# Kernel optimization log

Hardware: AMD Instinct MI355X
Metric: run time of the kernel (lower is better)

## Reference

```python
import jax, jax.numpy as jnp
import numpy as np

NEG_SLOPE = 0.2  # DGL GATConv default leaky_relu slope
N_LIG, E_LIG = 10000, 80000
N_REC, E_REC = 30000, 480000
B = 32  # graphs per batch


def setup_inputs() -> dict:
    key = jax.random.key(0)
    ks = jax.random.split(key, 32)
    d = {}
    d["x_lig"] = jax.random.normal(ks[0], (N_LIG, 64), jnp.float32)
    d["src_lig"] = jax.random.randint(ks[1], (E_LIG,), 0, N_LIG, jnp.int32)
    d["dst_lig"] = jax.random.randint(ks[2], (E_LIG,), 0, N_LIG, jnp.int32)
    d["gid_lig"] = jnp.sort(jax.random.randint(ks[3], (N_LIG,), 0, B, jnp.int32))
    d["x_rec"] = jax.random.normal(ks[4], (N_REC, 64), jnp.float32)
    d["src_rec"] = jax.random.randint(ks[5], (E_REC,), 0, N_REC, jnp.int32)
    d["dst_rec"] = jax.random.randint(ks[6], (E_REC,), 0, N_REC, jnp.int32)
    d["gid_rec"] = jnp.sort(jax.random.randint(ks[7], (N_REC,), 0, B, jnp.int32))
    s = 0.1
    # GAT layer 1 (lig): 64 -> 10 heads x 64 ; layer 2: 64 -> 1 head x 128
    d["W1l"] = s * jax.random.normal(ks[8], (64, 10 * 64), jnp.float32)
    d["al1l"] = s * jax.random.normal(ks[9], (10, 64), jnp.float32)
    d["ar1l"] = s * jax.random.normal(ks[10], (10, 64), jnp.float32)
    d["b1l"] = jnp.zeros((10, 64), jnp.float32)
    d["W2l"] = s * jax.random.normal(ks[11], (64, 128), jnp.float32)
    d["al2l"] = s * jax.random.normal(ks[12], (1, 128), jnp.float32)
    d["ar2l"] = s * jax.random.normal(ks[13], (1, 128), jnp.float32)
    d["b2l"] = jnp.zeros((1, 128), jnp.float32)
    d["W1r"] = s * jax.random.normal(ks[14], (64, 10 * 64), jnp.float32)
    d["al1r"] = s * jax.random.normal(ks[15], (10, 64), jnp.float32)
    d["ar1r"] = s * jax.random.normal(ks[16], (10, 64), jnp.float32)
    d["b1r"] = jnp.zeros((10, 64), jnp.float32)
    d["W2r"] = s * jax.random.normal(ks[17], (64, 128), jnp.float32)
    d["al2r"] = s * jax.random.normal(ks[18], (1, 128), jnp.float32)
    d["ar2r"] = s * jax.random.normal(ks[19], (1, 128), jnp.float32)
    d["b2r"] = jnp.zeros((1, 128), jnp.float32)
    d["W_lin1"] = s * jax.random.normal(ks[20], (256, 128), jnp.float32)
    d["b_lin1"] = jnp.zeros((128,), jnp.float32)
    d["W_lin2"] = s * jax.random.normal(ks[21], (128, 1), jnp.float32)
    d["b_lin2"] = jnp.zeros((1,), jnp.float32)
    return d


def gat_conv(x, src, dst, W, al, ar, b, num_nodes):
    # DGL GATConv (eval mode: dropouts off). al/ar: [H, D]
    H, D = al.shape
    h = (x @ W).reshape(num_nodes, H, D)          # [N, H, D]
    el = jnp.einsum("nhd,hd->nh", h, al)          # [N, H]
    er = jnp.einsum("nhd,hd->nh", h, ar)
    e = jax.nn.leaky_relu(el[src] + er[dst], NEG_SLOPE)   # [E, H]
    # edge softmax over incoming edges of each dst node
    emax = jax.ops.segment_max(e, dst, num_segments=num_nodes)
    ex = jnp.exp(e - emax[dst])
    denom = jax.ops.segment_sum(ex, dst, num_segments=num_nodes)
    alpha = ex / denom[dst]                       # [E, H]
    msg = alpha[:, :, None] * h[src]              # [E, H, D]
    out = jax.ops.segment_sum(msg, dst, num_segments=num_nodes)
    return out + b[None]                          # [N, H, D]


def branch(x, src, dst, gid, W1, al1, ar1, b1, W2, al2, ar2, b2):
    n = x.shape[0]
    h = jax.nn.relu(gat_conv(x, src, dst, W1, al1, ar1, b1, n)).sum(axis=1)  # sum heads -> [N, 64]
    h = jax.nn.relu(gat_conv(h, src, dst, W2, al2, ar2, b2, n))[:, 0, :]     # [N, 128]
    return jax.ops.segment_max(h, gid, num_segments=B)                       # max readout [B, 128]


def reference(x_lig, src_lig, dst_lig, gid_lig, x_rec, src_rec, dst_rec, gid_rec,
              W1l, al1l, ar1l, b1l, W2l, al2l, ar2l, b2l,
              W1r, al1r, ar1r, b1r, W2r, al2r, ar2r, b2r,
              W_lin1, b_lin1, W_lin2, b_lin2):
    hlig = branch(x_lig, src_lig, dst_lig, gid_lig, W1l, al1l, ar1l, b1l, W2l, al2l, ar2l, b2l)
    hrec = branch(x_rec, src_rec, dst_rec, gid_rec, W1r, al1r, ar1r, b1r, W2r, al2r, ar2r, b2r)
    h = jnp.concatenate([hlig, hrec], axis=-1)    # [B, 256]
    h = jax.nn.relu(h @ W_lin1 + b_lin1)
    h = jax.nn.relu(h @ W_lin2 + b_lin2)
    return h.flatten()                            # [B]
```

## Files before the change

### kernel.cpp

```cpp
#include <hip/hip_runtime.h>

#define LRELU(x) fmaxf((x), 0.2f*(x))
#define ZPAD(f) ((f) + 4*((f)>>6))

static inline int cdiv(int a, int b) { return (a + b - 1) / b; }

template<int H, int DH>
__global__ void prep_wal2_kernel(const float* __restrict__ WA, const float* __restrict__ alA,
                                 const float* __restrict__ arA, float* __restrict__ walA,
                                 float* __restrict__ warA, int nbA,
                                 const float* __restrict__ WB, const float* __restrict__ alB,
                                 const float* __restrict__ arB, float* __restrict__ walB,
                                 float* __restrict__ warB) {
  constexpr int K = 64;
  constexpr int HD = H * DH;
  const float *W, *al, *ar; float *wal, *war; int bid;
  if (blockIdx.x < (unsigned)nbA) { W=WA; al=alA; ar=arA; wal=walA; war=warA; bid=blockIdx.x; }
  else { W=WB; al=alB; ar=arB; wal=walB; war=warB; bid=blockIdx.x-nbA; }
  const int wv = threadIdx.x >> 6, lane = threadIdx.x & 63;
  const int o = bid * (blockDim.x >> 6) + wv;
  if (o >= H * K) return;
  const int h = o / K, k = o - h * K;
  float pl = 0.f, pr = 0.f;
#pragma unroll
  for (int j = 0; j < DH / 64; j++) {
    int d = j * 64 + lane;
    float w = W[(size_t)k * HD + h * DH + d];
    pl += w * al[h * DH + d];
    pr += w * ar[h * DH + d];
  }
#pragma unroll
  for (int off = 32; off >= 1; off >>= 1) {
    pl += __shfl_xor(pl, off);
    pr += __shfl_xor(pr, off);
  }
  if (lane == 0) { wal[o] = pl; war[o] = pr; }
}

__global__ void elr10_2_kernel(const float* __restrict__ xA, const float* __restrict__ walA,
                               const float* __restrict__ warA, float* __restrict__ elA,
                               float* __restrict__ erA, int NA, int nbA,
                               const float* __restrict__ xB, const float* __restrict__ walB,
                               const float* __restrict__ warB, float* __restrict__ elB,
                               float* __restrict__ erB, int NB) {
  const float *x, *wal, *war; float *el, *er; int N, bid;
  if (blockIdx.x < (unsigned)nbA) { x=xA; wal=walA; war=warA; el=elA; er=erA; N=NA; bid=blockIdx.x; }
  else { x=xB; wal=walB; war=warB; el=elB; er=erB; N=NB; bid=blockIdx.x-nbA; }
  const int wv = threadIdx.x >> 6, lane = threadIdx.x & 63;
  const int n = bid * (blockDim.x >> 6) + wv;
  if (n >= N) return;
  const float xv = x[(size_t)n * 64 + lane];
#pragma unroll
  for (int h = 0; h < 10; h++) {
    float pl = xv * wal[h * 64 + lane];
    float pr = xv * war[h * 64 + lane];
#pragma unroll
    for (int off = 32; off >= 1; off >>= 1) {
      pl += __shfl_xor(pl, off);
      pr += __shfl_xor(pr, off);
    }
    if (lane == 0) { el[(size_t)n * 10 + h] = pl; er[(size_t)n * 10 + h] = pr; }
  }
}

__global__ void deg2_kernel(const int* __restrict__ dstA, int* __restrict__ degA, int EA, int nbA,
                            const int* __restrict__ dstB, int* __restrict__ degB, int EB) {
  const int* dst; int* deg; int E, t;
  if (blockIdx.x < (unsigned)nbA) { dst=dstA; deg=degA; E=EA; t=blockIdx.x*256+threadIdx.x; }
  else { dst=dstB; deg=degB; E=EB; t=(blockIdx.x-nbA)*256+threadIdx.x; }
  if (t < E) atomicAdd(&deg[dst[t]], 1);
}

__global__ void rowptr2_kernel(const int* __restrict__ degA, int* __restrict__ rpA,
                               int* __restrict__ curA, int* __restrict__ cntA, int NA, int nbA,
                               const int* __restrict__ degB, int* __restrict__ rpB,
                               int* __restrict__ curB, int* __restrict__ cntB, int NB) {
  const int* deg; int *rp, *cur, *cnt; int N, t;
  if (blockIdx.x < (unsigned)nbA) { deg=degA; rp=rpA; cur=curA; cnt=cntA; N=NA; t=blockIdx.x*256+threadIdx.x; }
  else { deg=degB; rp=rpB; cur=curB; cnt=cntB; N=NB; t=(blockIdx.x-nbA)*256+threadIdx.x; }
  int lane = threadIdx.x & 63;
  int v = (t < N) ? deg[t] : 0;
  int x = v;
#pragma unroll
  for (int off = 1; off < 64; off <<= 1) {
    int y = __shfl_up(x, off);
    if (lane >= off) x += y;
  }
  int total = __shfl(x, 63);
  int base = 0;
  if (lane == 0 && total > 0) base = atomicAdd(cnt, total);
  base = __shfl(base, 0);
  int excl = base + x - v;
  if (t < N) { rp[t] = excl; cur[t] = excl; }
}

__global__ void scatter_ex2_kernel(
    const int* __restrict__ srcA, const int* __restrict__ dstA, int* __restrict__ curA,
    int* __restrict__ outA, const float* __restrict__ elA, const float* __restrict__ erA,
    float* __restrict__ exA, int EA, int nbA,
    const int* __restrict__ srcB, const int* __restrict__ dstB, int* __restrict__ curB,
    int* __restrict__ outB, const float* __restrict__ elB, const float* __restrict__ erB,
    float* __restrict__ exB, int EB) {
  const int *src, *dst; int *cur, *out; const float *el, *er; float *ex; int E, t;
  if (blockIdx.x < (unsigned)nbA) { src=srcA; dst=dstA; cur=curA; out=outA; el=elA; er=erA; ex=exA; E=EA; t=blockIdx.x*256+threadIdx.x; }
  else { src=srcB; dst=dstB; cur=curB; out=outB; el=elB; er=erB; ex=exB; E=EB; t=(blockIdx.x-nbA)*256+threadIdx.x; }
  if (t >= E) return;
  const int s = src[t], d = dst[t];
  const int slot = atomicAdd(&cur[d], 1);
  out[slot] = s;
  const float2* elv = (const float2*)el;
  const float2* erv = (const float2*)er;
  float2* exv = (float2*)ex;
#pragma unroll
  for (int j = 0; j < 5; j++) {
    float2 a = elv[(size_t)s * 5 + j];
    float2 b = erv[(size_t)d * 5 + j];
    float2 e;
    e.x = __expf(LRELU(a.x + b.x));
    e.y = __expf(LRELU(a.y + b.y));
    exv[(size_t)slot * 5 + j] = e;
  }
}

__global__ void aggr_z10_2_kernel(const int* __restrict__ rpA, const int* __restrict__ degA,
                                  const int* __restrict__ srcsA, const float* __restrict__ xA,
                                  const float* __restrict__ exA, float* __restrict__ zA,
                                  int NA, int nbA,
                                  const int* __restrict__ rpB, const int* __restrict__ degB,
                                  const int* __restrict__ srcsB, const float* __restrict__ xB,
                                  const float* __restrict__ exB, float* __restrict__ zB, int NB) {
  const int *rp, *degp, *srcs; const float *x, *ex; float *z; int N, bid;
  if (blockIdx.x < (unsigned)nbA) { rp=rpA; degp=degA; srcs=srcsA; x=xA; ex=exA; z=zA; N=NA; bid=blockIdx.x; }
  else { rp=rpB; degp=degB; srcs=srcsB; x=xB; ex=exB; z=zB; N=NB; bid=blockIdx.x-nbA; }
  const int wv = threadIdx.x >> 6, lane = threadIdx.x & 63;
  const int n = bid * (blockDim.x >> 6) + wv;
  if (n >= N) return;
  const int beg = rp[n], dg = degp[n];
  const float2* exv = (const float2*)ex;
  float den[10], acc[10];
#pragma unroll
  for (int h = 0; h < 10; h++) { den[h] = 0.f; acc[h] = 0.f; }
  int i = 0;
  for (; i + 1 < dg; i += 2) {
    int s0 = srcs[beg + i], s1 = srcs[beg + i + 1];
    float xv0 = x[(size_t)s0 * 64 + lane];
    float xv1 = x[(size_t)s1 * 64 + lane];
    float e0[10], e1[10];
#pragma unroll
    for (int j = 0; j < 5; j++) {
      float2 a = exv[(size_t)(beg + i) * 5 + j];
      float2 c = exv[(size_t)(beg + i + 1) * 5 + j];
      e0[2 * j] = a.x; e0[2 * j + 1] = a.y;
      e1[2 * j] = c.x; e1[2 * j + 1] = c.y;
    }
#pragma unroll
    for (int h = 0; h < 10; h++) {
      den[h] += e0[h] + e1[h];
      acc[h] = fmaf(e0[h], xv0, fmaf(e1[h], xv1, acc[h]));
    }
  }
  if (i < dg) {
    int s0 = srcs[beg + i];
    float xv0 = x[(size_t)s0 * 64 + lane];
#pragma unroll
    for (int j = 0; j < 5; j++) {
      float2 a = exv[(size_t)(beg + i) * 5 + j];
      den[2 * j] += a.x;
      den[2 * j + 1] += a.y;
      acc[2 * j] = fmaf(a.x, xv0, acc[2 * j]);
      acc[2 * j + 1] = fmaf(a.y, xv0, acc[2 * j + 1]);
    }
  }
#pragma unroll
  for (int h = 0; h < 10; h++)
    z[(size_t)n * 640 + h * 64 + lane] = (dg > 0) ? acc[h] / den[h] : 0.f;
}

__global__ void aggr_z1_2_kernel(const int* __restrict__ rpA, const int* __restrict__ degA,
                                 const int* __restrict__ srcsA, const float* __restrict__ hA,
                                 const float* __restrict__ elA, const float* __restrict__ erA,
                                 float* __restrict__ zA, int NA, int nbA,
                                 const int* __restrict__ rpB, const int* __restrict__ degB,
                                 const int* __restrict__ srcsB, const float* __restrict__ hB,
                                 const float* __restrict__ elB, const float* __restrict__ erB,
                                 float* __restrict__ zB, int NB) {
  const int *rp, *degp, *srcs; const float *hin, *el, *er; float *z; int N, bid;
  if (blockIdx.x < (unsigned)nbA) { rp=rpA; degp=degA; srcs=srcsA; hin=hA; el=elA; er=erA; z=zA; N=NA; bid=blockIdx.x; }
  else { rp=rpB; degp=degB; srcs=srcsB; hin=hB; el=elB; er=erB; z=zB; N=NB; bid=blockIdx.x-nbA; }
  const int wv = threadIdx.x >> 6, lane = threadIdx.x & 63;
  const int n = bid * (blockDim.x >> 6) + wv;
  if (n >= N) return;
  const int beg = rp[n], dg = degp[n];
  const float ern = er[n];
  float den = 0.f, acc = 0.f;
  int i = 0;
  for (; i + 1 < dg; i += 2) {
    int s0 = srcs[beg + i], s1 = srcs[beg + i + 1];
    float x0 = __expf(LRELU(el[s0] + ern));
    float x1 = __expf(LRELU(el[s1] + ern));
    den += x0 + x1;
    acc += x0 * hin[(size_t)s0 * 64 + lane] + x1 * hin[(size_t)s1 * 64 + lane];
  }
  if (i < dg) {
    int s0 = srcs[beg + i];
    float x0 = __expf(LRELU(el[s0] + ern));
    den += x0;
    acc += x0 * hin[(size_t)s0 * 64 + lane];
  }
  z[(size_t)n * 64 + lane] = (dg > 0) ? acc / den : 0.f;
}

__global__ void gemm_sumheads2_kernel(
    const float* __restrict__ zA, const float* __restrict__ WA, const float* __restrict__ bA,
    const float* __restrict__ wal2A, const float* __restrict__ war2A, float* __restrict__ h1A,
    float* __restrict__ el2A, float* __restrict__ er2A, int NA, int nbA,
    const float* __restrict__ zB, const float* __restrict__ WB, const float* __restrict__ bB,
    const float* __restrict__ wal2B, const float* __restrict__ war2B, float* __restrict__ h1B,
    float* __restrict__ el2B, float* __restrict__ er2B, int NB) {
  constexpr int NPB = 16;
  __shared__ float zs[NPB][680];
  const float *z, *W, *bb, *wal2, *war2; float *h1sum, *el2, *er2; int N, tile;
  if (blockIdx.x < (unsigned)nbA) { z=zA; W=WA; bb=bA; wal2=wal2A; war2=war2A; h1sum=h1A; el2=el2A; er2=er2A; N=NA; tile=blockIdx.x; }
  else { z=zB; W=WB; bb=bB; wal2=wal2B; war2=war2B; h1sum=h1B; el2=el2B; er2=er2B; N=NB; tile=blockIdx.x-nbA; }
  const int f = threadIdx.x;
  const int n0 = tile * NPB;
  const int pf = ZPAD(f);
#pragma unroll
  for (int i = 0; i < NPB; i++) {
    int n = n0 + i;
    zs[i][pf] = (n < N) ? z[(size_t)n * 640 + f] : 0.f;
  }
  __syncthreads();
  const int f4 = f % 160;
  const int ng = f / 160;
  const int head = f4 >> 4;
  const int base = 68 * head;
  float acc[4][4];
#pragma unroll
  for (int i = 0; i < 4; i++)
#pragma unroll
    for (int j = 0; j < 4; j++) acc[i][j] = 0.f;
  const float4* W4 = (const float4*)W;
#pragma unroll 4
  for (int k4 = 0; k4 < 16; k4++) {
    float4 zq[4];
#pragma unroll
    for (int i = 0; i < 4; i++)
      zq[i] = *(const float4*)&zs[ng * 4 + i][base + 4 * k4];
#pragma unroll
    for (int j4 = 0; j4 < 4; j4++) {
      const int k = 4 * k4 + j4;
      const float4 w4 = W4[(size_t)k * 160 + f4];
#pragma unroll
      for (int i = 0; i < 4; i++) {
        const float zv = j4 == 0 ? zq[i].x : j4 == 1 ? zq[i].y : j4 == 2 ? zq[i].z : zq[i].w;
        acc[i][0] = fmaf(zv, w4.x, acc[i][0]);
        acc[i][1] = fmaf(zv, w4.y, acc[i][1]);
        acc[i][2] = fmaf(zv, w4.z, acc[i][2]);
        acc[i][3] = fmaf(zv, w4.w, acc[i][3]);
      }
    }
  }
  const float4 b4 = ((const float4*)bb)[f4];
  __syncthreads();
#pragma unroll
  for (int i = 0; i < 4; i++) {
    float* row = &zs[ng * 4 + i][ZPAD(4 * f4)];
    row[0] = fmaxf(acc[i][0] + b4.x, 0.f);
    row[1] = fmaxf(acc[i][1] + b4.y, 0.f);
    row[2] = fmaxf(acc[i][2] + b4.z, 0.f);
    row[3] = fmaxf(acc[i][3] + b4.w, 0.f);
  }
  __syncthreads();
  const int lane = threadIdx.x & 63;
  for (int idx = threadIdx.x; idx < NPB * 64; idx += 640) {
    const int i = idx >> 6, d = idx & 63;
    float s = 0.f;
#pragma unroll
    for (int h = 0; h < 10; h++) s += zs[i][68 * h + d];
    const int n = n0 + i;
    float pl = s * wal2[d], pr = s * war2[d];
#pragma unroll
    for (int off = 32; off >= 1; off >>= 1) {
      pl += __shfl_xor(pl, off);
      pr += __shfl_xor(pr, off);
    }
    if (n < N) {
      h1sum[(size_t)n * 64 + d] = s;
      if (lane == 0) { el2[n] = pl; er2[n] = pr; }
    }
  }
}

__global__ void gemm2_readout3_kernel(
    const float* __restrict__ zA, const float* __restrict__ WA, const float* __restrict__ bA,
    const int* __restrict__ gidA, int NA, int coA, int nbA,
    const float* __restrict__ zB, const float* __restrict__ WB, const float* __restrict__ bB,
    const int* __restrict__ gidB, int NB, int coB,
    float* __restrict__ readout) {
  constexpr int NPB = 16;
  __shared__ float zs[NPB][64];
  __shared__ float vals[NPB][128];
  __shared__ int gids[NPB];
  const float *z, *W, *bb; const int* gid; int N, colOff, tile;
  if (blockIdx.x < (unsigned)nbA) { z=zA; W=WA; bb=bA; gid=gidA; N=NA; colOff=coA; tile=blockIdx.x; }
  else { z=zB; W=WB; bb=bB; gid=gidB; N=NB; colOff=coB; tile=blockIdx.x-nbA; }
  const int f = threadIdx.x;
  const int n0 = tile * NPB;
  for (int idx = f; idx < NPB * 64; idx += 128) {
    int i = idx >> 6, k = idx & 63;
    int n = n0 + i;
    zs[i][k] = (n < N) ? z[(size_t)n * 64 + k] : 0.f;
  }
  if (f < NPB) gids[f] = (n0 + f < N) ? gid[n0 + f] : -1;
  __syncthreads();
  float acc[NPB];
#pragma unroll
  for (int i = 0; i < NPB; i++) acc[i] = 0.f;
#pragma unroll 4
  for (int k4 = 0; k4 < 16; k4++) {
    const float w0 = W[(size_t)(4 * k4 + 0) * 128 + f];
    const float w1 = W[(size_t)(4 * k4 + 1) * 128 + f];
    const float w2 = W[(size_t)(4 * k4 + 2) * 128 + f];
    const float w3 = W[(size_t)(4 * k4 + 3) * 128 + f];
#pragma unroll
    for (int i = 0; i < NPB; i++) {
      float4 zq = *(const float4*)&zs[i][4 * k4];
      acc[i] = fmaf(zq.x, w0, fmaf(zq.y, w1, fmaf(zq.z, w2, fmaf(zq.w, w3, acc[i]))));
    }
  }
  const float bbf = bb[f];
#pragma unroll
  for (int i = 0; i < NPB; i++) vals[i][f] = fmaxf(acc[i] + bbf, 0.f);
  __syncthreads();
  float run = 0.f;
  int curg = -1;
#pragma unroll
  for (int i = 0; i < NPB; i++) {
    int g = gids[i];
    if (g < 0) break;
    if (g != curg) {
      if (curg >= 0)
        atomicMax((unsigned int*)&readout[curg * 256 + colOff + f], __float_as_uint(run));
      curg = g;
      run = 0.f;
    }
    run = fmaxf(run, vals[i][f]);
  }
  if (curg >= 0)
    atomicMax((unsigned int*)&readout[curg * 256 + colOff + f], __float_as_uint(run));
}

__global__ void mlp_kernel(const float* __restrict__ readout, const float* __restrict__ W1,
                           const float* __restrict__ b1, const float* __restrict__ W2,
                           const float* __restrict__ b2, float* __restrict__ out) {
  int b = blockIdx.x;
  int j = threadIdx.x;
  __shared__ float rs[256];
  rs[j] = readout[b * 256 + j];
  rs[j + 128] = readout[b * 256 + 128 + j];
  __syncthreads();
  float acc = b1[j];
#pragma unroll 8
  for (int k = 0; k < 256; k++) acc += rs[k] * W1[k * 128 + j];
  acc = fmaxf(acc, 0.f);
  float p = acc * W2[j];
#pragma unroll
  for (int off = 32; off >= 1; off >>= 1) p += __shfl_xor(p, off);
  __shared__ float wsum[2];
  if ((threadIdx.x & 63) == 0) wsum[threadIdx.x >> 6] = p;
  __syncthreads();
  if (threadIdx.x == 0) {
    float s = wsum[0] + wsum[1] + b2[0];
    out[b] = fmaxf(s, 0.f);
  }
}

extern "C" void kernel_launch(void* const* d_in, const int* in_sizes, int n_in,
                              void* d_out, int out_size, void* d_ws, size_t ws_size,
                              hipStream_t stream) {
  const float* x_lig = (const float*)d_in[0];
  const int* src_lig = (const int*)d_in[1];
  const int* dst_lig = (const int*)d_in[2];
  const int* gid_lig = (const int*)d_in[3];
  const float* x_rec = (const float*)d_in[4];
  const int* src_rec = (const int*)d_in[5];
  const int* dst_rec = (const int*)d_in[6];
  const int* gid_rec = (const int*)d_in[7];
  const float* W1l = (const float*)d_in[8];
  const float* al1l = (const float*)d_in[9];
  const float* ar1l = (const float*)d_in[10];
  const float* b1l = (const float*)d_in[11];
  const float* W2l = (const float*)d_in[12];
  const float* al2l = (const float*)d_in[13];
  const float* ar2l = (const float*)d_in[14];
  const float* b2l = (const float*)d_in[15];
  const float* W1r = (const float*)d_in[16];
  const float* al1r = (const float*)d_in[17];
  const float* ar1r = (const float*)d_in[18];
  const float* b1r = (const float*)d_in[19];
  const float* W2r = (const float*)d_in[20];
  const float* al2r = (const float*)d_in[21];
  const float* ar2r = (const float*)d_in[22];
  const float* b2r = (const float*)d_in[23];
  const float* W_lin1 = (const float*)d_in[24];
  const float* b_lin1 = (const float*)d_in[25];
  const float* W_lin2 = (const float*)d_in[26];
  const float* b_lin2 = (const float*)d_in[27];

  const int NL = 10000, EL = 80000, NR = 30000, ER = 480000;
  float* p = (float*)d_ws;
  float* zL = p;      p += (size_t)NL * 640;
  float* zR = p;      p += (size_t)NR * 640;
  float* ex1L = p;    p += (size_t)EL * 10;
  float* ex1R = p;    p += (size_t)ER * 10;
  float* z2L = p;     p += (size_t)NL * 64;
  float* z2R = p;     p += (size_t)NR * 64;
  float* h1L = p;     p += (size_t)NL * 64;
  float* h1R = p;     p += (size_t)NR * 64;
  float* el1L = p;    p += (size_t)NL * 10;
  float* er1L = p;    p += (size_t)NL * 10;
  float* el1R = p;    p += (size_t)NR * 10;
  float* er1R = p;    p += (size_t)NR * 10;
  float* el2L = p;    p += NL;
  float* er2L = p;    p += NL;
  float* el2R = p;    p += NR;
  float* er2R = p;    p += NR;
  float* wal1l = p;   p += 640;
  float* war1l = p;   p += 640;
  float* wal1r = p;   p += 640;
  float* war1r = p;   p += 640;
  float* wal2l = p;   p += 64;
  float* war2l = p;   p += 64;
  float* wal2r = p;   p += 64;
  float* war2r = p;   p += 64;
  float* zero_base = p;
  float* readout = p; p += 32 * 256;
  int* ip = (int*)p;
  int* degL = ip;     ip += NL;
  int* cntL = ip;     ip += 1;
  int* degR = ip;     ip += NR;
  int* cntR = ip;     ip += 1;
  size_t zero_bytes = (size_t)((char*)ip - (char*)zero_base);
  int* rpL = ip;      ip += NL;
  int* curL = ip;     ip += NL;
  int* srcsL = ip;    ip += EL;
  int* rpR = ip;      ip += NR;
  int* curR = ip;     ip += NR;
  int* srcsR = ip;    ip += ER;

  hipMemsetAsync(zero_base, 0, zero_bytes, stream);

  prep_wal2_kernel<10, 64><<<160, 512, 0, stream>>>(W1l, al1l, ar1l, wal1l, war1l, 80,
                                                    W1r, al1r, ar1r, wal1r, war1r);
  prep_wal2_kernel<1, 128><<<16, 512, 0, stream>>>(W2l, al2l, ar2l, wal2l, war2l, 8,
                                                   W2r, al2r, ar2r, wal2r, war2r);
  deg2_kernel<<<cdiv(EL, 256) + cdiv(ER, 256), 256, 0, stream>>>(
      dst_lig, degL, EL, cdiv(EL, 256), dst_rec, degR, ER);
  rowptr2_kernel<<<cdiv(NL, 256) + cdiv(NR, 256), 256, 0, stream>>>(
      degL, rpL, curL, cntL, NL, cdiv(NL, 256), degR, rpR, curR, cntR, NR);
  elr10_2_kernel<<<cdiv(NL, 4) + cdiv(NR, 4), 256, 0, stream>>>(
      x_lig, wal1l, war1l, el1L, er1L, NL, cdiv(NL, 4),
      x_rec, wal1r, war1r, el1R, er1R, NR);
  scatter_ex2_kernel<<<cdiv(EL, 256) + cdiv(ER, 256), 256, 0, stream>>>(
      src_lig, dst_lig, curL, srcsL, el1L, er1L, ex1L, EL, cdiv(EL, 256),
      src_rec, dst_rec, curR, srcsR, el1R, er1R, ex1R, ER);
  aggr_z10_2_kernel<<<cdiv(NL, 8) + cdiv(NR, 8), 512, 0, stream>>>(
      rpL, degL, srcsL, x_lig, ex1L, zL, NL, cdiv(NL, 8),
      rpR, degR, srcsR, x_rec, ex1R, zR, NR);
  gemm_sumheads2_kernel<<<cdiv(NL, 16) + cdiv(NR, 16), 640, 0, stream>>>(
      zL, W1l, b1l, wal2l, war2l, h1L, el2L, er2L, NL, cdiv(NL, 16),
      zR, W1r, b1r, wal2r, war2r, h1R, el2R, er2R, NR);
  aggr_z1_2_kernel<<<cdiv(NL, 8) + cdiv(NR, 8), 512, 0, stream>>>(
      rpL, degL, srcsL, h1L, el2L, er2L, z2L, NL, cdiv(NL, 8),
      rpR, degR, srcsR, h1R, el2R, er2R, z2R, NR);
  gemm2_readout3_kernel<<<cdiv(NL, 16) + cdiv(NR, 16), 128, 0, stream>>>(
      z2L, W2l, b2l, gid_lig, NL, 0, cdiv(NL, 16),
      z2R, W2r, b2r, gid_rec, NR, 128, readout);

  mlp_kernel<<<32, 128, 0, stream>>>(readout, W_lin1, b_lin1, W_lin2, b_lin2, (float*)d_out);
}
```

Measured before the change: 494.6 us.

## Precompute layer-2 edge attention exps in separate kernel and prefetch GEMM weights

The layer-2 attention exponentials move out of the aggregation loop into a new per-edge kernel. It writes them in CSR slot order, using a slot map recorded during the scatter. This removes the random el gathers and expf calls from the warp-per-node aggregation, at the cost of an extra kernel launch and extra edge-sized buffers. The sum-heads GEMM also double-buffers its W float4 loads in registers to overlap global loads with FMAs, which raises register pressure.

```diff
diff --git a/kernel.cpp b/kernel.cpp
--- a/kernel.cpp
+++ b/kernel.cpp
@@ -97,17 +97,18 @@
 __global__ void scatter_ex2_kernel(
     const int* __restrict__ srcA, const int* __restrict__ dstA, int* __restrict__ curA,
     int* __restrict__ outA, const float* __restrict__ elA, const float* __restrict__ erA,
-    float* __restrict__ exA, int EA, int nbA,
+    float* __restrict__ exA, int* __restrict__ eslotA, int EA, int nbA,
     const int* __restrict__ srcB, const int* __restrict__ dstB, int* __restrict__ curB,
     int* __restrict__ outB, const float* __restrict__ elB, const float* __restrict__ erB,
-    float* __restrict__ exB, int EB) {
-  const int *src, *dst; int *cur, *out; const float *el, *er; float *ex; int E, t;
-  if (blockIdx.x < (unsigned)nbA) { src=srcA; dst=dstA; cur=curA; out=outA; el=elA; er=erA; ex=exA; E=EA; t=blockIdx.x*256+threadIdx.x; }
-  else { src=srcB; dst=dstB; cur=curB; out=outB; el=elB; er=erB; ex=exB; E=EB; t=(blockIdx.x-nbA)*256+threadIdx.x; }
+    float* __restrict__ exB, int* __restrict__ eslotB, int EB) {
+  const int *src, *dst; int *cur, *out, *eslot; const float *el, *er; float *ex; int E, t;
+  if (blockIdx.x < (unsigned)nbA) { src=srcA; dst=dstA; cur=curA; out=outA; el=elA; er=erA; ex=exA; eslot=eslotA; E=EA; t=blockIdx.x*256+threadIdx.x; }
+  else { src=srcB; dst=dstB; cur=curB; out=outB; el=elB; er=erB; ex=exB; eslot=eslotB; E=EB; t=(blockIdx.x-nbA)*256+threadIdx.x; }
   if (t >= E) return;
   const int s = src[t], d = dst[t];
   const int slot = atomicAdd(&cur[d], 1);
   out[slot] = s;
+  eslot[t] = slot;
   const float2* elv = (const float2*)el;
   const float2* erv = (const float2*)er;
   float2* exv = (float2*)ex;
@@ -120,6 +121,20 @@
     e.y = __expf(LRELU(a.y + b.y));
     exv[(size_t)slot * 5 + j] = e;
   }
+}
+
+__global__ void ex2_2_kernel(const int* __restrict__ srcA, const int* __restrict__ dstA,
+                             const int* __restrict__ eslotA, const float* __restrict__ el2A,
+                             const float* __restrict__ er2A, float* __restrict__ ex2A,
+                             int EA, int nbA,
+                             const int* __restrict__ srcB, const int* __restrict__ dstB,
+                             const int* __restrict__ eslotB, const float* __restrict__ el2B,
+                             const float* __restrict__ er2B, float* __restrict__ ex2B, int EB) {
+  const int *src, *dst, *eslot; const float *el2, *er2; float *ex2; int E, t;
+  if (blockIdx.x < (unsigned)nbA) { src=srcA; dst=dstA; eslot=eslotA; el2=el2A; er2=er2A; ex2=ex2A; E=EA; t=blockIdx.x*256+threadIdx.x; }
+  else { src=srcB; dst=dstB; eslot=eslotB; el2=el2B; er2=er2B; ex2=ex2B; E=EB; t=(blockIdx.x-nbA)*256+threadIdx.x; }
+  if (t >= E) return;
+  ex2[eslot[t]] = __expf(LRELU(el2[src[t]] + er2[dst[t]]));
 }
 
 __global__ void aggr_z10_2_kernel(const int* __restrict__ rpA, const int* __restrict__ degA,
@@ -178,34 +193,31 @@
 
 __global__ void aggr_z1_2_kernel(const int* __restrict__ rpA, const int* __restrict__ degA,
                                  const int* __restrict__ srcsA, const float* __restrict__ hA,
-                                 const float* __restrict__ elA, const float* __restrict__ erA,
-                                 float* __restrict__ zA, int NA, int nbA,
+                                 const float* __restrict__ exA, float* __restrict__ zA,
+                                 int NA, int nbA,
                                  const int* __restrict__ rpB, const int* __restrict__ degB,
                                  const int* __restrict__ srcsB, const float* __restrict__ hB,
-                                 const float* __restrict__ elB, const float* __restrict__ erB,
-                                 float* __restrict__ zB, int NB) {
-  const int *rp, *degp, *srcs; const float *hin, *el, *er; float *z; int N, bid;
-  if (blockIdx.x < (unsigned)nbA) { rp=rpA; degp=degA; srcs=srcsA; hin=hA; el=elA; er=erA; z=zA; N=NA; bid=blockIdx.x; }
-  else { rp=rpB; degp=degB; srcs=srcsB; hin=hB; el=elB; er=erB; z=zB; N=NB; bid=blockIdx.x-nbA; }
+                                 const float* __restrict__ exB, float* __restrict__ zB, int NB) {
+  const int *rp, *degp, *srcs; const float *hin, *ex; float *z; int N, bid;
+  if (blockIdx.x < (unsigned)nbA) { rp=rpA; degp=degA; srcs=srcsA; hin=hA; ex=exA; z=zA; N=NA; bid=blockIdx.x; }
+  else { rp=rpB; degp=degB; srcs=srcsB; hin=hB; ex=exB; z=zB; N=NB; bid=blockIdx.x-nbA; }
   const int wv = threadIdx.x >> 6, lane = threadIdx.x & 63;
   const int n = bid * (blockDim.x >> 6) + wv;
   if (n >= N) return;
   const int beg = rp[n], dg = degp[n];
-  const float ern = er[n];
   float den = 0.f, acc = 0.f;
   int i = 0;
   for (; i + 1 < dg; i += 2) {
     int s0 = srcs[beg + i], s1 = srcs[beg + i + 1];
-    float x0 = __expf(LRELU(el[s0] + ern));
-    float x1 = __expf(LRELU(el[s1] + ern));
-    den += x0 + x1;
-    acc += x0 * hin[(size_t)s0 * 64 + lane] + x1 * hin[(size_t)s1 * 64 + lane];
+    float e0 = ex[beg + i], e1 = ex[beg + i + 1];
+    den += e0 + e1;
+    acc = fmaf(e0, hin[(size_t)s0 * 64 + lane], fmaf(e1, hin[(size_t)s1 * 64 + lane], acc));
   }
   if (i < dg) {
     int s0 = srcs[beg + i];
-    float x0 = __expf(LRELU(el[s0] + ern));
-    den += x0;
-    acc += x0 * hin[(size_t)s0 * 64 + lane];
+    float e0 = ex[beg + i];
+    den += e0;
+    acc = fmaf(e0, hin[(size_t)s0 * 64 + lane], acc);
   }
   z[(size_t)n * 64 + lane] = (dg > 0) ? acc / den : 0.f;
 }
@@ -241,16 +253,25 @@
 #pragma unroll
     for (int j = 0; j < 4; j++) acc[i][j] = 0.f;
   const float4* W4 = (const float4*)W;
-#pragma unroll 4
+  float4 wn[4];
+#pragma unroll
+  for (int j = 0; j < 4; j++) wn[j] = W4[(size_t)j * 160 + f4];
+#pragma unroll
   for (int k4 = 0; k4 < 16; k4++) {
+    float4 wc[4];
+#pragma unroll
+    for (int j = 0; j < 4; j++) wc[j] = wn[j];
+    if (k4 < 15) {
+#pragma unroll
+      for (int j = 0; j < 4; j++) wn[j] = W4[(size_t)(4 * (k4 + 1) + j) * 160 + f4];
+    }
     float4 zq[4];
 #pragma unroll
     for (int i = 0; i < 4; i++)
       zq[i] = *(const float4*)&zs[ng * 4 + i][base + 4 * k4];
 #pragma unroll
     for (int j4 = 0; j4 < 4; j4++) {
-      const int k = 4 * k4 + j4;
-      const float4 w4 = W4[(size_t)k * 160 + f4];
+      const float4 w4 = wc[j4];
 #pragma unroll
       for (int i = 0; i < 4; i++) {
         const float zv = j4 == 0 ? zq[i].x : j4 == 1 ? zq[i].y : j4 == 2 ? zq[i].z : zq[i].w;
@@ -414,6 +435,8 @@
   float* zR = p;      p += (size_t)NR * 640;
   float* ex1L = p;    p += (size_t)EL * 10;
   float* ex1R = p;    p += (size_t)ER * 10;
+  float* ex2L = p;    p += EL;
+  float* ex2R = p;    p += ER;
   float* z2L = p;     p += (size_t)NL * 64;
   float* z2R = p;     p += (size_t)NR * 64;
   float* h1L = p;     p += (size_t)NL * 64;
@@ -448,6 +471,8 @@
   int* rpR = ip;      ip += NR;
   int* curR = ip;     ip += NR;
   int* srcsR = ip;    ip += ER;
+  int* eslotL = ip;   ip += EL;
+  int* eslotR = ip;   ip += ER;
 
   hipMemsetAsync(zero_base, 0, zero_bytes, stream);
 
@@ -463,17 +488,20 @@
       x_lig, wal1l, war1l, el1L, er1L, NL, cdiv(NL, 4),
       x_rec, wal1r, war1r, el1R, er1R, NR);
   scatter_ex2_kernel<<<cdiv(EL, 256) + cdiv(ER, 256), 256, 0, stream>>>(
-      src_lig, dst_lig, curL, srcsL, el1L, er1L, ex1L, EL, cdiv(EL, 256),
-      src_rec, dst_rec, curR, srcsR, el1R, er1R, ex1R, ER);
+      src_lig, dst_lig, curL, srcsL, el1L, er1L, ex1L, eslotL, EL, cdiv(EL, 256),
+      src_rec, dst_rec, curR, srcsR, el1R, er1R, ex1R, eslotR, ER);
   aggr_z10_2_kernel<<<cdiv(NL, 8) + cdiv(NR, 8), 512, 0, stream>>>(
       rpL, degL, srcsL, x_lig, ex1L, zL, NL, cdiv(NL, 8),
       rpR, degR, srcsR, x_rec, ex1R, zR, NR);
   gemm_sumheads2_kernel<<<cdiv(NL, 16) + cdiv(NR, 16), 640, 0, stream>>>(
       zL, W1l, b1l, wal2l, war2l, h1L, el2L, er2L, NL, cdiv(NL, 16),
       zR, W1r, b1r, wal2r, war2r, h1R, el2R, er2R, NR);
+  ex2_2_kernel<<<cdiv(EL, 256) + cdiv(ER, 256), 256, 0, stream>>>(
+      src_lig, dst_lig, eslotL, el2L, er2L, ex2L, EL, cdiv(EL, 256),
+      src_rec, dst_rec, eslotR, el2R, er2R, ex2R, ER);
   aggr_z1_2_kernel<<<cdiv(NL, 8) + cdiv(NR, 8), 512, 0, stream>>>(
-      rpL, degL, srcsL, h1L, el2L, er2L, z2L, NL, cdiv(NL, 8),
-      rpR, degR, srcsR, h1R, el2R, er2R, z2R, NR);
+      rpL, degL, srcsL, h1L, ex2L, z2L, NL, cdiv(NL, 8),
+      rpR, degR, srcsR, h1R, ex2R, z2R, NR);
   gemm2_readout3_kernel<<<cdiv(NL, 16) + cdiv(NR, 16), 128, 0, stream>>>(
       z2L, W2l, b2l, gid_lig, NL, 0, cdiv(NL, 16),
       z2R, W2r, b2r, gid_rec, NR, 128, readout);
```

Result: faster. 480.1 us (-2.9%).
